# Kernel optimization log

Measured on AMD Instinct MI355X. Metric: run time of the kernel, lower is better.

Reference implementation:

```python
import jax, jax.numpy as jnp
import numpy as np

B, S, H, D = 2, 4096, 16, 128  # batch, seq, heads, head_dim
HID = H * D                    # 2048 hidden size
C = 128                        # chunk size for the chunked recurrent scan
EPS = 1e-6


def setup_inputs() -> dict:
    key = jax.random.key(0)
    ks = jax.random.split(key, 9)
    sc = 0.02  # initializer_range
    w = lambda k: jax.random.normal(k, (HID, HID), jnp.float32) * sc
    return {
        "x": jax.random.normal(ks[0], (B, S, HID), jnp.float32),
        "Wq": w(ks[1]), "bq": jnp.zeros((HID,), jnp.float32),
        "Wk": w(ks[2]), "bk": jnp.zeros((HID,), jnp.float32),
        "Wv": w(ks[3]), "bv": jnp.zeros((HID,), jnp.float32),
        "Wo": w(ks[4]), "bo": jnp.zeros((HID,), jnp.float32),
    }


def reference(x, Wq, bq, Wk, bk, Wv, bv, Wo, bo):
    Bx, Sx, hid = x.shape
    NC = Sx // C  # number of chunks

    q = (x @ Wq + bq).reshape(Bx, Sx, H, D)
    k = (x @ Wk + bk).reshape(Bx, Sx, H, D)
    v = (x @ Wv + bv).reshape(Bx, Sx, H, D)

    # positive feature map for linear attention
    qf = jax.nn.elu(q) + 1.0
    kf = jax.nn.elu(k) + 1.0

    # chunk: [B, NC, C, H, D]
    qf = qf.reshape(Bx, NC, C, H, D)
    kf = kf.reshape(Bx, NC, C, H, D)
    vc = v.reshape(Bx, NC, C, H, D)

    # inter-chunk recurrent state: exclusive cumulative sums of per-chunk KV outer
    kv = jnp.einsum('bnchd,bnche->bnhde', kf, vc)      # per-chunk KV state
    kv_ex = jnp.cumsum(kv, axis=1) - kv                # exclusive prefix state
    ksum = kf.sum(axis=2)                              # [B,NC,H,D]
    ksum_ex = jnp.cumsum(ksum, axis=1) - ksum          # exclusive normalizer state

    inter = jnp.einsum('bnchd,bnhde->bnche', qf, kv_ex)
    z_inter = jnp.einsum('bnchd,bnhd->bnch', qf, ksum_ex)

    # intra-chunk causal attention (masked matmul)
    A = jnp.einsum('bnchd,bnkhd->bnhck', qf, kf)       # [B,NC,H,C,C]
    causal = jnp.tril(jnp.ones((C, C), dtype=bool))
    A = jnp.where(causal[None, None, None], A, 0.0)
    intra = jnp.einsum('bnhck,bnkhe->bnche', A, vc)
    z_intra = jnp.swapaxes(A.sum(-1), 2, 3)            # [B,NC,C,H]

    out = (inter + intra) / (z_inter + z_intra + EPS)[..., None]
    out = out.reshape(Bx, Sx, hid)
    return out @ Wo + bo
```

## Files before the change

### kernel.cpp

```cpp
#include <hip/hip_runtime.h>

typedef unsigned short u16;
typedef unsigned int u32;
typedef unsigned long long u64;
typedef __attribute__((ext_vector_type(8))) short short8;
typedef __attribute__((ext_vector_type(4))) float f32x4;
typedef __attribute__((ext_vector_type(4))) int int4v;

constexpr int Bsz = 2, Ssz = 4096, Hn = 16, Dh = 128, HID = 2048;
constexpr int Cch = 128, NCh = 32;
constexpr float EPSf = 1e-6f;

#define MFMA16 __builtin_amdgcn_mfma_f32_16x16x32_bf16
#define VMW(N) asm volatile("s_waitcnt vmcnt(" #N ")" ::: "memory")

__device__ __forceinline__ float b2f(u16 u) {
  unsigned int i = ((unsigned int)u) << 16;
  return __builtin_bit_cast(float, i);
}
__device__ __forceinline__ u16 f2b(float f) {
  unsigned int i = __builtin_bit_cast(unsigned int, f);
  i += 0x7fffu + ((i >> 16) & 1u);
  return (u16)(i >> 16);
}

__device__ __forceinline__ void gload_lds16(const u16* g, u16* l) {
  __builtin_amdgcn_global_load_lds(
      (const __attribute__((address_space(1))) u32*)g,
      (__attribute__((address_space(3))) u32*)l, 16, 0, 0);
}

__global__ __launch_bounds__(256) void cvt_bf16(const float* __restrict__ x,
                                                u16* __restrict__ xb)
{
  const size_t n8 = (size_t)Bsz * Ssz * HID / 8;
  for (size_t i = (size_t)blockIdx.x * 256 + threadIdx.x; i < n8;
       i += (size_t)gridDim.x * 256) {
    const f32x4 a = *(const f32x4*)&x[i * 8];
    const f32x4 b = *(const f32x4*)&x[i * 8 + 4];
    u16 tmp[8];
#pragma unroll
    for (int u = 0; u < 4; ++u) { tmp[u] = f2b(a[u]); tmp[u + 4] = f2b(b[u]); }
    *(int4v*)&xb[i * 8] = *(const int4v*)tmp;
  }
}

__global__ __launch_bounds__(256) void transpose4(
    const float* __restrict__ A0, const float* __restrict__ A1,
    const float* __restrict__ A2, const float* __restrict__ A3,
    u16* __restrict__ T0, u16* __restrict__ T1,
    u16* __restrict__ T2, u16* __restrict__ T3)
{
  constexpr int N = HID, LDT = 72;
  const int z = blockIdx.z;
  const float* __restrict__ A = (z == 0) ? A0 : (z == 1) ? A1 : (z == 2) ? A2 : A3;
  u16* __restrict__ T = (z == 0) ? T0 : (z == 1) ? T1 : (z == 2) ? T2 : T3;
  __shared__ u16 lds[64 * LDT];
  const int t = threadIdx.x;
  const int i = t >> 3, j = (t & 7) * 8;
  const int r0 = blockIdx.y * 64, c0 = blockIdx.x * 64;
#pragma unroll
  for (int half = 0; half < 2; ++half) {
    const int r = i + half * 32;
    const f32x4 a = *(const f32x4*)&A[(size_t)(r0 + r) * N + c0 + j];
    const f32x4 b = *(const f32x4*)&A[(size_t)(r0 + r) * N + c0 + j + 4];
    u16 tmp[8];
#pragma unroll
    for (int u = 0; u < 4; ++u) { tmp[u] = f2b(a[u]); tmp[u + 4] = f2b(b[u]); }
    *(int4v*)&lds[r * LDT + j] = *(const int4v*)tmp;
  }
  __syncthreads();
#pragma unroll
  for (int half = 0; half < 2; ++half) {
    const int c = i + half * 32;
    u16 tmp[8];
#pragma unroll
    for (int u = 0; u < 8; ++u) tmp[u] = lds[(j + u) * LDT + c];
    *(int4v*)&T[(size_t)(c0 + c) * N + r0 + j] = *(const int4v*)tmp;
  }
}

template <int OUTF32>
__global__ __launch_bounds__(512) void gemm4b(
    const u16* __restrict__ A,
    const u16* __restrict__ W0T, const u16* __restrict__ W1T, const u16* __restrict__ W2T,
    const float* __restrict__ bb0, const float* __restrict__ bb1, const float* __restrict__ bb2,
    void* __restrict__ o0, void* __restrict__ o1, void* __restrict__ o2,
    int elu_mask)
{
  constexpr int K = HID, N = HID;
  extern __shared__ u16 lds[];

  const int z = blockIdx.z;
  const u16* __restrict__ WT    = (z == 0) ? W0T : (z == 1) ? W1T : W2T;
  const float* __restrict__ bias = (z == 0) ? bb0 : (z == 1) ? bb1 : bb2;
  void* __restrict__ outv = (z == 0) ? o0 : (z == 1) ? o1 : o2;
  const bool elu = (elu_mask >> z) & 1;

  const int lid = blockIdx.x + 8 * blockIdx.y;
  const int k8 = lid & 7, j32 = lid >> 3;
  const int m0 = (k8 * 4 + (j32 >> 3)) * 256;
  const int n0 = (j32 & 7) * 256;

  const int t = threadIdx.x, lane = t & 63, w = t >> 6;
  const int wm = w >> 2, wn = w & 3;
  const int l15 = lane & 15, lg = lane >> 4;
  const int sl2 = (l15 >> 1) & 3;

  const int strow = lane >> 2;
  const int stslot = (lane & 3) ^ ((lane >> 3) & 3);
  const u16* gA = A  + (size_t)(m0 + w * 16 + strow) * K + stslot * 8;
  const u16* gB = WT + (size_t)(n0 + w * 16 + strow) * K + stslot * 8;

  const int aRow = (wm * 128 + l15) * 32 + ((lg ^ sl2) << 3);
  const int bRow = 8192 + (wn * 64 + l15) * 32 + ((lg ^ sl2) << 3);
  u16* const lw = &lds[w * 512];

  f32x4 acc[8][4] = {};
  short8 aF[8], bF[4];

#define STAGE4(SB) do {                                                       \
    gload_lds16(gA,                   lw + (SB)*16384);                       \
    gload_lds16(gA + (size_t)128*K,   lw + (SB)*16384 + 4096);                \
    gload_lds16(gB,                   lw + (SB)*16384 + 8192);                \
    gload_lds16(gB + (size_t)128*K,   lw + (SB)*16384 + 8192 + 4096);         \
    gA += 32; gB += 32;                                                       \
  } while (0)

#define WINDOW(BUF, SB, PF, VMN) do {                                         \
    VMW(VMN);                                                                 \
    __builtin_amdgcn_s_barrier();                                             \
    if (PF) STAGE4(SB);                                                       \
    _Pragma("unroll")                                                         \
    for (int i = 0; i < 8; ++i)                                               \
      aF[i] = *(const short8*)&lds[(BUF)*16384 + aRow + i*512];               \
    _Pragma("unroll")                                                         \
    for (int j = 0; j < 4; ++j)                                               \
      bF[j] = *(const short8*)&lds[(BUF)*16384 + bRow + j*512];               \
    __builtin_amdgcn_s_setprio(1);                                            \
    _Pragma("unroll")                                                         \
    for (int i = 0; i < 8; ++i) {                                             \
      acc[i][0] = MFMA16(aF[i], bF[0], acc[i][0], 0, 0, 0);                   \
      acc[i][1] = MFMA16(aF[i], bF[1], acc[i][1], 0, 0, 0);                   \
      acc[i][2] = MFMA16(aF[i], bF[2], acc[i][2], 0, 0, 0);                   \
      acc[i][3] = MFMA16(aF[i], bF[3], acc[i][3], 0, 0, 0);                   \
    }                                                                         \
    __builtin_amdgcn_s_setprio(0);                                            \
  } while (0)

  STAGE4(0);
  STAGE4(1);
  STAGE4(2);

  for (int W = 0; W < 60; W += 4) {
    WINDOW(0, 3, 1, 8);
    WINDOW(1, 0, 1, 8);
    WINDOW(2, 1, 1, 8);
    WINDOW(3, 2, 1, 8);
  }
  WINDOW(0, 3, 1, 8);
  WINDOW(1, 0, 0, 8);
  WINDOW(2, 0, 0, 4);
  WINDOW(3, 0, 0, 0);

  if (OUTF32) {
#pragma unroll
    for (int j = 0; j < 4; ++j) {
      const int col = n0 + wn * 64 + j * 16 + l15;
      const float bv = bias[col];
#pragma unroll
      for (int i = 0; i < 8; ++i) {
        const int row0 = m0 + wm * 128 + i * 16 + lg * 4;
#pragma unroll
        for (int r = 0; r < 4; ++r) {
          float v = acc[i][j][r] + bv;
          if (elu) v = (v > 0.0f) ? (v + 1.0f) : __expf(v);
          ((float*)outv)[(size_t)(row0 + r) * N + col] = v;
        }
      }
    }
  } else {
    __builtin_amdgcn_s_barrier();
    u16* const myr = &lds[w * 8192];
#pragma unroll
    for (int j = 0; j < 4; ++j) {
      const float bv = bias[n0 + wn * 64 + j * 16 + l15];
#pragma unroll
      for (int i = 0; i < 8; ++i)
#pragma unroll
        for (int r = 0; r < 4; ++r) {
          float v = acc[i][j][r] + bv;
          if (elu) v = (v > 0.0f) ? (v + 1.0f) : __expf(v);
          myr[(i * 16 + lg * 4 + r) * 64 + j * 16 + l15] = f2b(v);
        }
    }
    const int rl = lane >> 3, ch = (lane & 7) * 8;
    u16* const og = (u16*)outv + (size_t)(m0 + wm * 128) * N + n0 + wn * 64;
#pragma unroll
    for (int si = 0; si < 16; ++si) {
      const int rw = si * 8 + rl;
      *(int4v*)&og[(size_t)rw * N + ch] = *(const int4v*)&myr[rw * 64 + ch];
    }
  }
#undef STAGE4
#undef WINDOW
}

__global__ __launch_bounds__(256) void pass1_kv(
    const u16* __restrict__ KF, const u16* __restrict__ V,
    u16* __restrict__ KVT, float* __restrict__ KSUM)
{
  constexpr int LD = 136;
  __shared__ u16 lk[128 * LD];
  __shared__ u16 lv[128 * LD];
  __shared__ float kp[256];
  const int bnh = blockIdx.x;
  const int h = bnh % Hn, n = (bnh / Hn) % NCh, b = bnh / (Hn * NCh);
  const size_t rowbase = (size_t)(b * Ssz + n * Cch) * HID + h * Dh;
  const int t = threadIdx.x, lane = t & 63, w = t >> 6;
  const int wr = (w >> 1) * 64, wc = (w & 1) * 64;
  const int l15 = lane & 15, lg = lane >> 4;
  const int sr = t >> 4, sc = (t & 15) * 8;

#pragma unroll
  for (int rep = 0; rep < 8; ++rep) {
    const int r = rep * 16 + sr;
    *(int4v*)&lk[r * LD + sc] = *(const int4v*)&KF[rowbase + (size_t)r * HID + sc];
    *(int4v*)&lv[r * LD + sc] = *(const int4v*)&V[rowbase + (size_t)r * HID + sc];
  }
  __syncthreads();

  {
    const int col = t & 127, hf = t >> 7;
    float s = 0.0f;
    for (int c = hf * 64; c < hf * 64 + 64; ++c) s += b2f(lk[c * LD + col]);
    kp[t] = s;
  }
  __syncthreads();
  if (t < 128) KSUM[(size_t)bnh * Dh + t] = kp[t] + kp[t + 128];

  f32x4 acc[4][4] = {};
#pragma unroll
  for (int kk = 0; kk < 4; ++kk) {
    const int cb = kk * 32 + lg * 8;
    short8 aF[4], bF[4];
#pragma unroll
    for (int i = 0; i < 4; ++i) {
      const int e = wr + i * 16 + l15;
      short8 a;
#pragma unroll
      for (int u = 0; u < 8; ++u) a[u] = (short)lv[(cb + u) * LD + e];
      aF[i] = a;
    }
#pragma unroll
    for (int j = 0; j < 4; ++j) {
      const int d = wc + j * 16 + l15;
      short8 bb;
#pragma unroll
      for (int u = 0; u < 8; ++u) bb[u] = (short)lk[(cb + u) * LD + d];
      bF[j] = bb;
    }
#pragma unroll
    for (int i = 0; i < 4; ++i)
#pragma unroll
      for (int j = 0; j < 4; ++j)
        acc[i][j] = MFMA16(aF[i], bF[j], acc[i][j], 0, 0, 0);
  }

  u16* __restrict__ outp = KVT + (size_t)bnh * (Dh * Dh);
#pragma unroll
  for (int i = 0; i < 4; ++i) {
    const int e0 = wr + i * 16 + lg * 4;
#pragma unroll
    for (int j = 0; j < 4; ++j) {
      const int d = wc + j * 16 + l15;
#pragma unroll
      for (int r = 0; r < 4; ++r)
        outp[(size_t)(e0 + r) * Dh + d] = f2b(acc[i][j][r]);
    }
  }
}

__global__ __launch_bounds__(256) void cumsum_all(u16* __restrict__ KVT,
                                                  float* __restrict__ KS)
{
  const int nkv = (Bsz * Hn * Dh * Dh) / 256;
  if ((int)blockIdx.x < nkv) {
    const int tid = blockIdx.x * 256 + threadIdx.x;
    const int ed = tid & (Dh * Dh - 1);
    const int bh = tid >> 14;
    const int h = bh % Hn, b = bh / Hn;
    const size_t base = ((size_t)(b * NCh * Hn) + h) * (Dh * Dh) + ed;
    const size_t stride = (size_t)Hn * Dh * Dh;
    float s = 0.0f;
    for (int n = 0; n < NCh; ++n) {
      const size_t idx = base + (size_t)n * stride;
      const float v = b2f(KVT[idx]);
      KVT[idx] = f2b(s);
      s += v;
    }
  } else {
    const int tid = (blockIdx.x - nkv) * 256 + threadIdx.x;
    const int d = tid & (Dh - 1);
    const int bh = tid >> 7;
    const int h = bh % Hn, b = bh / Hn;
    const size_t base = ((size_t)(b * NCh * Hn) + h) * Dh + d;
    const size_t stride = (size_t)Hn * Dh;
    float s = 0.0f;
    for (int n = 0; n < NCh; ++n) {
      const size_t idx = base + (size_t)n * stride;
      const float v = KS[idx];
      KS[idx] = s;
      s += v;
    }
  }
}

__global__ __launch_bounds__(256) void pass2_attn(
    const u16* __restrict__ QF, const u16* __restrict__ KF, const u16* __restrict__ V,
    const u16* __restrict__ KVT, const float* __restrict__ KSE,
    u16* __restrict__ Y)
{
  constexpr int LD = 136;
  __shared__ u16 smem[4 * 128 * LD];
  __shared__ float zpart[2][128];
  u16* sQ  = smem;
  u16* sK  = smem + 128 * LD;
  u16* sA  = smem + 2 * 128 * LD;
  u16* sKV = smem + 3 * 128 * LD;

  const int bnh = blockIdx.x;
  const int h = bnh % Hn, n = (bnh / Hn) % NCh, b = bnh / (Hn * NCh);
  const size_t rowbase = (size_t)(b * Ssz + n * Cch) * HID + h * Dh;
  const int t = threadIdx.x, lane = t & 63, w = t >> 6;
  const int wr = (w >> 1) * 64, wc = (w & 1) * 64;
  const int l15 = lane & 15, lg = lane >> 4;
  const int sr = t >> 4, sc = (t & 15) * 8;

  const u16* __restrict__ kvsrc = KVT + (size_t)bnh * (Dh * Dh);
#pragma unroll
  for (int rep = 0; rep < 8; ++rep) {
    const int r = rep * 16 + sr;
    *(int4v*)&sQ[r * LD + sc]  = *(const int4v*)&QF[rowbase + (size_t)r * HID + sc];
    *(int4v*)&sK[r * LD + sc]  = *(const int4v*)&KF[rowbase + (size_t)r * HID + sc];
    *(int4v*)&sKV[r * LD + sc] = *(const int4v*)&kvsrc[r * Dh + sc];
  }
  __syncthreads();

  f32x4 acc[4][4] = {};
#pragma unroll
  for (int kk = 0; kk < 4; ++kk) {
    const int krd = kk * 32 + lg * 8;
    short8 aF[4], bF[4];
#pragma unroll
    for (int i = 0; i < 4; ++i)
      aF[i] = *(const short8*)&sQ[(wr + i * 16 + l15) * LD + krd];
#pragma unroll
    for (int j = 0; j < 4; ++j)
      bF[j] = *(const short8*)&sK[(wc + j * 16 + l15) * LD + krd];
#pragma unroll
    for (int i = 0; i < 4; ++i)
#pragma unroll
      for (int j = 0; j < 4; ++j)
        acc[i][j] = MFMA16(aF[i], bF[j], acc[i][j], 0, 0, 0);
  }
#pragma unroll
  for (int i = 0; i < 4; ++i) {
    const int c0 = wr + i * 16 + lg * 4;
#pragma unroll
    for (int j = 0; j < 4; ++j) {
      const int ck = wc + j * 16 + l15;
#pragma unroll
      for (int r = 0; r < 4; ++r) {
        const int c = c0 + r;
        sA[c * LD + ck] = f2b((ck <= c) ? acc[i][j][r] : 0.0f);
      }
    }
  }
  __syncthreads();

  if (t < 128) {
    const float* kse = KSE + (size_t)bnh * Dh;
    float zz = 0.0f;
    for (int d2 = 0; d2 < 128; d2 += 8) {
      const short8 q8 = *(const short8*)&sQ[t * LD + d2];
      const f32x4 k0 = *(const f32x4*)&kse[d2];
      const f32x4 k1 = *(const f32x4*)&kse[d2 + 4];
      zz += b2f((u16)q8[0]) * k0[0] + b2f((u16)q8[1]) * k0[1]
          + b2f((u16)q8[2]) * k0[2] + b2f((u16)q8[3]) * k0[3]
          + b2f((u16)q8[4]) * k1[0] + b2f((u16)q8[5]) * k1[1]
          + b2f((u16)q8[6]) * k1[2] + b2f((u16)q8[7]) * k1[3];
    }
    zpart[0][t] = zz;
  } else {
    const int row = t - 128;
    float zz = 0.0f;
    for (int ck = 0; ck < 128; ck += 8) {
      const short8 a8 = *(const short8*)&sA[row * LD + ck];
#pragma unroll
      for (int u = 0; u < 8; ++u) zz += b2f((u16)a8[u]);
    }
    zpart[1][row] = zz;
  }
#pragma unroll
  for (int rep = 0; rep < 8; ++rep) {
    const int r = rep * 16 + sr;
    *(int4v*)&sK[r * LD + sc] = *(const int4v*)&V[rowbase + (size_t)r * HID + sc];
  }
  __syncthreads();

  f32x4 o[4][4] = {};
#pragma unroll
  for (int kk = 0; kk < 4; ++kk) {
    const int krd = kk * 32 + lg * 8;
    short8 aF[4], bF[4];
#pragma unroll
    for (int i = 0; i < 4; ++i)
      aF[i] = *(const short8*)&sA[(wr + i * 16 + l15) * LD + krd];
#pragma unroll
    for (int j = 0; j < 4; ++j) {
      const int e = wc + j * 16 + l15;
      short8 bb;
#pragma unroll
      for (int u = 0; u < 8; ++u) bb[u] = (short)sK[(krd + u) * LD + e];
      bF[j] = bb;
    }
#pragma unroll
    for (int i = 0; i < 4; ++i)
#pragma unroll
      for (int j = 0; j < 4; ++j)
        o[i][j] = MFMA16(aF[i], bF[j], o[i][j], 0, 0, 0);
  }
#pragma unroll
  for (int kk = 0; kk < 4; ++kk) {
    const int krd = kk * 32 + lg * 8;
    short8 aF[4], bF[4];
#pragma unroll
    for (int i = 0; i < 4; ++i)
      aF[i] = *(const short8*)&sQ[(wr + i * 16 + l15) * LD + krd];
#pragma unroll
    for (int j = 0; j < 4; ++j)
      bF[j] = *(const short8*)&sKV[(wc + j * 16 + l15) * LD + krd];
#pragma unroll
    for (int i = 0; i < 4; ++i)
#pragma unroll
      for (int j = 0; j < 4; ++j)
        o[i][j] = MFMA16(aF[i], bF[j], o[i][j], 0, 0, 0);
  }

#pragma unroll
  for (int i = 0; i < 4; ++i) {
    const int c0 = wr + i * 16 + lg * 4;
#pragma unroll
    for (int j = 0; j < 4; ++j) {
      const int e = wc + j * 16 + l15;
#pragma unroll
      for (int r = 0; r < 4; ++r) {
        const int c = c0 + r;
        const float zz = zpart[0][c] + zpart[1][c] + EPSf;
        Y[rowbase + (size_t)c * HID + e] = f2b(o[i][j][r] / zz);
      }
    }
  }
}

extern "C" void kernel_launch(void* const* d_in, const int* in_sizes, int n_in,
                              void* d_out, int out_size, void* d_ws, size_t ws_size,
                              hipStream_t stream)
{
  const float* x  = (const float*)d_in[0];
  const float* Wq = (const float*)d_in[1];
  const float* bq = (const float*)d_in[2];
  const float* Wk = (const float*)d_in[3];
  const float* bk = (const float*)d_in[4];
  const float* Wv = (const float*)d_in[5];
  const float* bv = (const float*)d_in[6];
  const float* Wo = (const float*)d_in[7];
  const float* bo = (const float*)d_in[8];
  float* out = (float*)d_out;

  char* p = (char*)d_ws;
  auto take = [&](size_t bytes) { char* q = p; p += (bytes + 255) & ~(size_t)255; return q; };
  u16* WqT = (u16*)take((size_t)HID * HID * 2);
  u16* WkT = (u16*)take((size_t)HID * HID * 2);
  u16* WvT = (u16*)take((size_t)HID * HID * 2);
  u16* WoT = (u16*)take((size_t)HID * HID * 2);
  u16* QF  = (u16*)take((size_t)Bsz * Ssz * HID * 2);
  u16* KFb = (u16*)take((size_t)Bsz * Ssz * HID * 2);
  u16* Vb  = (u16*)take((size_t)Bsz * Ssz * HID * 2);
  char* region = take((size_t)Bsz * Ssz * HID * 2);
  u16* xb  = (u16*)region;
  u16* KVT = (u16*)region;
  float* KS = (float*)take((size_t)Bsz * NCh * Hn * Dh * 4);
  u16* Yb = QF;

  (void)hipFuncSetAttribute((const void*)gemm4b<0>,
                            hipFuncAttributeMaxDynamicSharedMemorySize, 131072);
  (void)hipFuncSetAttribute((const void*)gemm4b<1>,
                            hipFuncAttributeMaxDynamicSharedMemorySize, 131072);

  dim3 blk(256, 1, 1);
  cvt_bf16<<<dim3(2048), blk, 0, stream>>>(x, xb);
  transpose4<<<dim3(HID / 64, HID / 64, 4), blk, 0, stream>>>(
      Wq, Wk, Wv, Wo, WqT, WkT, WvT, WoT);
  gemm4b<0><<<dim3(HID / 256, (Bsz * Ssz) / 256, 3), dim3(512), 131072, stream>>>(
      xb, WqT, WkT, WvT, bq, bk, bv, QF, KFb, Vb, 0x3);
  pass1_kv<<<dim3(Bsz * NCh * Hn), blk, 0, stream>>>(KFb, Vb, KVT, KS);
  cumsum_all<<<dim3((Bsz * Hn * Dh * Dh) / 256 + (Bsz * Hn * Dh) / 256), blk, 0, stream>>>(KVT, KS);
  pass2_attn<<<dim3(Bsz * NCh * Hn), blk, 0, stream>>>(QF, KFb, Vb, KVT, KS, Yb);
  gemm4b<1><<<dim3(HID / 256, (Bsz * Ssz) / 256, 1), dim3(512), 131072, stream>>>(
      Yb, WoT, WoT, WoT, bo, bo, bo, out, out, out, 0);
}
```

Before: 387.3 us.

## Merge prep kernels and stage attention-pass outputs through LDS for coalesced stores

Folds the fp32-to-bf16 input conversion into the weight-transpose kernel as an extra grid slice, removing one launch. In pass1_kv and pass2_attn, MFMA accumulator results are first written to shared memory and then stored to global memory as 16-byte row-contiguous vectors, replacing scattered 2-byte stores. This trades extra barriers and LDS traffic for far fewer, wider global writes.

```diff
diff --git a/kernel.cpp b/kernel.cpp
--- a/kernel.cpp
+++ b/kernel.cpp
@@ -30,22 +30,8 @@
       (__attribute__((address_space(3))) u32*)l, 16, 0, 0);
 }
 
-__global__ __launch_bounds__(256) void cvt_bf16(const float* __restrict__ x,
-                                                u16* __restrict__ xb)
-{
-  const size_t n8 = (size_t)Bsz * Ssz * HID / 8;
-  for (size_t i = (size_t)blockIdx.x * 256 + threadIdx.x; i < n8;
-       i += (size_t)gridDim.x * 256) {
-    const f32x4 a = *(const f32x4*)&x[i * 8];
-    const f32x4 b = *(const f32x4*)&x[i * 8 + 4];
-    u16 tmp[8];
-#pragma unroll
-    for (int u = 0; u < 4; ++u) { tmp[u] = f2b(a[u]); tmp[u + 4] = f2b(b[u]); }
-    *(int4v*)&xb[i * 8] = *(const int4v*)tmp;
-  }
-}
-
-__global__ __launch_bounds__(256) void transpose4(
+__global__ __launch_bounds__(256) void prep(
+    const float* __restrict__ x, u16* __restrict__ xb,
     const float* __restrict__ A0, const float* __restrict__ A1,
     const float* __restrict__ A2, const float* __restrict__ A3,
     u16* __restrict__ T0, u16* __restrict__ T1,
@@ -53,10 +39,25 @@
 {
   constexpr int N = HID, LDT = 72;
   const int z = blockIdx.z;
+  const int t = threadIdx.x;
+
+  if (z == 4) {
+    const size_t n8 = (size_t)Bsz * Ssz * HID / 8;
+    const int bid = blockIdx.y * 32 + blockIdx.x;
+    for (size_t i = (size_t)bid * 256 + t; i < n8; i += (size_t)1024 * 256) {
+      const f32x4 a = *(const f32x4*)&x[i * 8];
+      const f32x4 b = *(const f32x4*)&x[i * 8 + 4];
+      u16 tmp[8];
+#pragma unroll
+      for (int u = 0; u < 4; ++u) { tmp[u] = f2b(a[u]); tmp[u + 4] = f2b(b[u]); }
+      *(int4v*)&xb[i * 8] = *(const int4v*)tmp;
+    }
+    return;
+  }
+
   const float* __restrict__ A = (z == 0) ? A0 : (z == 1) ? A1 : (z == 2) ? A2 : A3;
   u16* __restrict__ T = (z == 0) ? T0 : (z == 1) ? T1 : (z == 2) ? T2 : T3;
   __shared__ u16 lds[64 * LDT];
-  const int t = threadIdx.x;
   const int i = t >> 3, j = (t & 7) * 8;
   const int r0 = blockIdx.y * 64, c0 = blockIdx.x * 64;
 #pragma unroll
@@ -267,7 +268,7 @@
         acc[i][j] = MFMA16(aF[i], bF[j], acc[i][j], 0, 0, 0);
   }
 
-  u16* __restrict__ outp = KVT + (size_t)bnh * (Dh * Dh);
+  __syncthreads();
 #pragma unroll
   for (int i = 0; i < 4; ++i) {
     const int e0 = wr + i * 16 + lg * 4;
@@ -276,8 +277,17 @@
       const int d = wc + j * 16 + l15;
 #pragma unroll
       for (int r = 0; r < 4; ++r)
-        outp[(size_t)(e0 + r) * Dh + d] = f2b(acc[i][j][r]);
-    }
+        lv[(e0 + r) * LD + d] = f2b(acc[i][j][r]);
+    }
+  }
+  __syncthreads();
+  {
+    u16* __restrict__ outp = KVT + (size_t)bnh * (Dh * Dh);
+    const int row = t >> 1, half = (t & 1) * 64;
+#pragma unroll
+    for (int c8 = 0; c8 < 8; ++c8)
+      *(int4v*)&outp[(size_t)row * Dh + half + c8 * 8] =
+          *(const int4v*)&lv[row * LD + half + c8 * 8];
   }
 }
 
@@ -448,6 +458,7 @@
         o[i][j] = MFMA16(aF[i], bF[j], o[i][j], 0, 0, 0);
   }
 
+  __syncthreads();
 #pragma unroll
   for (int i = 0; i < 4; ++i) {
     const int c0 = wr + i * 16 + lg * 4;
@@ -458,9 +469,17 @@
       for (int r = 0; r < 4; ++r) {
         const int c = c0 + r;
         const float zz = zpart[0][c] + zpart[1][c] + EPSf;
-        Y[rowbase + (size_t)c * HID + e] = f2b(o[i][j][r] / zz);
+        sA[c * LD + e] = f2b(o[i][j][r] / zz);
       }
     }
+  }
+  __syncthreads();
+  {
+    const int row = t >> 1, half = (t & 1) * 64;
+#pragma unroll
+    for (int c8 = 0; c8 < 8; ++c8)
+      *(int4v*)&Y[rowbase + (size_t)row * HID + half + c8 * 8] =
+          *(const int4v*)&sA[row * LD + half + c8 * 8];
   }
 }
 
@@ -500,9 +519,8 @@
                             hipFuncAttributeMaxDynamicSharedMemorySize, 131072);
 
   dim3 blk(256, 1, 1);
-  cvt_bf16<<<dim3(2048), blk, 0, stream>>>(x, xb);
-  transpose4<<<dim3(HID / 64, HID / 64, 4), blk, 0, stream>>>(
-      Wq, Wk, Wv, Wo, WqT, WkT, WvT, WoT);
+  prep<<<dim3(32, 32, 5), blk, 0, stream>>>(
+      x, xb, Wq, Wk, Wv, Wo, WqT, WkT, WvT, WoT);
   gemm4b<0><<<dim3(HID / 256, (Bsz * Ssz) / 256, 3), dim3(512), 131072, stream>>>(
       xb, WqT, WkT, WvT, bq, bk, bv, QF, KFb, Vb, 0x3);
   pass1_kv<<<dim3(Bsz * NCh * Hn), blk, 0, stream>>>(KFb, Vb, KVT, KS);
```

After: 398.5 us. 2.9% more time.

## Use 4-wave GEMM blocks with 128x128 per-wave tiles

Applied to the files above, without the earlier changes.

The projection GEMM drops from 8 waves per 256x256 block to 4 waves, each computing a 128x128 sub-tile with 64 accumulators. This doubles register-level reuse of A/B fragments per LDS read and reduces LDS read traffic per MFMA. In exchange, register pressure rises sharply (256 accumulator floats per lane) and there are fewer waves to hide latency, so occupancy drops and spilling is possible.

```diff
diff --git a/kernel.cpp b/kernel.cpp
--- a/kernel.cpp
+++ b/kernel.cpp
@@ -81,7 +81,7 @@
 }
 
 template <int OUTF32>
-__global__ __launch_bounds__(512) void gemm4b(
+__global__ __launch_bounds__(256, 1) void gemm4w(
     const u16* __restrict__ A,
     const u16* __restrict__ W0T, const u16* __restrict__ W1T, const u16* __restrict__ W2T,
     const float* __restrict__ bb0, const float* __restrict__ bb1, const float* __restrict__ bb2,
@@ -103,70 +103,70 @@
   const int n0 = (j32 & 7) * 256;
 
   const int t = threadIdx.x, lane = t & 63, w = t >> 6;
-  const int wm = w >> 2, wn = w & 3;
+  const int wm = w >> 1, wn = w & 1;
   const int l15 = lane & 15, lg = lane >> 4;
   const int sl2 = (l15 >> 1) & 3;
 
   const int strow = lane >> 2;
   const int stslot = (lane & 3) ^ ((lane >> 3) & 3);
-  const u16* gA = A  + (size_t)(m0 + w * 16 + strow) * K + stslot * 8;
-  const u16* gB = WT + (size_t)(n0 + w * 16 + strow) * K + stslot * 8;
+  const u16* gA = A  + (size_t)(m0 + w * 64 + strow) * K + stslot * 8;
+  const u16* gB = WT + (size_t)(n0 + w * 64 + strow) * K + stslot * 8;
 
   const int aRow = (wm * 128 + l15) * 32 + ((lg ^ sl2) << 3);
-  const int bRow = 8192 + (wn * 64 + l15) * 32 + ((lg ^ sl2) << 3);
-  u16* const lw = &lds[w * 512];
-
-  f32x4 acc[8][4] = {};
-  short8 aF[8], bF[4];
-
-#define STAGE4(SB) do {                                                       \
-    gload_lds16(gA,                   lw + (SB)*16384);                       \
-    gload_lds16(gA + (size_t)128*K,   lw + (SB)*16384 + 4096);                \
-    gload_lds16(gB,                   lw + (SB)*16384 + 8192);                \
-    gload_lds16(gB + (size_t)128*K,   lw + (SB)*16384 + 8192 + 4096);         \
+  const int bRow = 8192 + (wn * 128 + l15) * 32 + ((lg ^ sl2) << 3);
+  u16* const lw = &lds[w * 2048];
+
+  f32x4 acc[8][8] = {};
+  short8 aF[8], bF[8];
+
+#define STAGE8(SB) do {                                                       \
+    _Pragma("unroll")                                                         \
+    for (int q = 0; q < 4; ++q)                                               \
+      gload_lds16(gA + (size_t)(q * 16) * K, lw + (SB)*16384 + q * 512);      \
+    _Pragma("unroll")                                                         \
+    for (int q = 0; q < 4; ++q)                                               \
+      gload_lds16(gB + (size_t)(q * 16) * K, lw + (SB)*16384 + 8192 + q * 512);\
     gA += 32; gB += 32;                                                       \
   } while (0)
 
 #define WINDOW(BUF, SB, PF, VMN) do {                                         \
     VMW(VMN);                                                                 \
     __builtin_amdgcn_s_barrier();                                             \
-    if (PF) STAGE4(SB);                                                       \
+    if (PF) STAGE8(SB);                                                       \
     _Pragma("unroll")                                                         \
     for (int i = 0; i < 8; ++i)                                               \
       aF[i] = *(const short8*)&lds[(BUF)*16384 + aRow + i*512];               \
     _Pragma("unroll")                                                         \
-    for (int j = 0; j < 4; ++j)                                               \
+    for (int j = 0; j < 8; ++j)                                               \
       bF[j] = *(const short8*)&lds[(BUF)*16384 + bRow + j*512];               \
     __builtin_amdgcn_s_setprio(1);                                            \
     _Pragma("unroll")                                                         \
-    for (int i = 0; i < 8; ++i) {                                             \
-      acc[i][0] = MFMA16(aF[i], bF[0], acc[i][0], 0, 0, 0);                   \
-      acc[i][1] = MFMA16(aF[i], bF[1], acc[i][1], 0, 0, 0);                   \
-      acc[i][2] = MFMA16(aF[i], bF[2], acc[i][2], 0, 0, 0);                   \
-      acc[i][3] = MFMA16(aF[i], bF[3], acc[i][3], 0, 0, 0);                   \
-    }                                                                         \
+    for (int i = 0; i < 8; ++i)                                               \
+      _Pragma("unroll")                                                       \
+      for (int j = 0; j < 8; ++j)                                             \
+        acc[i][j] = MFMA16(aF[i], bF[j], acc[i][j], 0, 0, 0);                 \
     __builtin_amdgcn_s_setprio(0);                                            \
   } while (0)
 
-  STAGE4(0);
-  STAGE4(1);
-  STAGE4(2);
+  STAGE8(0);
+  STAGE8(1);
+  STAGE8(2);
 
   for (int W = 0; W < 60; W += 4) {
-    WINDOW(0, 3, 1, 8);
-    WINDOW(1, 0, 1, 8);
-    WINDOW(2, 1, 1, 8);
-    WINDOW(3, 2, 1, 8);
-  }
-  WINDOW(0, 3, 1, 8);
-  WINDOW(1, 0, 0, 8);
-  WINDOW(2, 0, 0, 4);
+    WINDOW(0, 3, 1, 16);
+    WINDOW(1, 0, 1, 16);
+    WINDOW(2, 1, 1, 16);
+    WINDOW(3, 2, 1, 16);
+  }
+  WINDOW(0, 3, 1, 16);
+  WINDOW(1, 0, 0, 16);
+  WINDOW(2, 0, 0, 8);
   WINDOW(3, 0, 0, 0);
 
   if (OUTF32) {
 #pragma unroll
-    for (int j = 0; j < 4; ++j) {
-      const int col = n0 + wn * 64 + j * 16 + l15;
+    for (int j = 0; j < 8; ++j) {
+      const int col = n0 + wn * 128 + j * 16 + l15;
       const float bv = bias[col];
 #pragma unroll
       for (int i = 0; i < 8; ++i) {
@@ -181,28 +181,28 @@
     }
   } else {
     __builtin_amdgcn_s_barrier();
-    u16* const myr = &lds[w * 8192];
-#pragma unroll
-    for (int j = 0; j < 4; ++j) {
-      const float bv = bias[n0 + wn * 64 + j * 16 + l15];
+    u16* const myr = &lds[w * 16384];
+#pragma unroll
+    for (int j = 0; j < 8; ++j) {
+      const float bv = bias[n0 + wn * 128 + j * 16 + l15];
 #pragma unroll
       for (int i = 0; i < 8; ++i)
 #pragma unroll
         for (int r = 0; r < 4; ++r) {
           float v = acc[i][j][r] + bv;
           if (elu) v = (v > 0.0f) ? (v + 1.0f) : __expf(v);
-          myr[(i * 16 + lg * 4 + r) * 64 + j * 16 + l15] = f2b(v);
+          myr[(i * 16 + lg * 4 + r) * 128 + j * 16 + l15] = f2b(v);
         }
     }
-    const int rl = lane >> 3, ch = (lane & 7) * 8;
-    u16* const og = (u16*)outv + (size_t)(m0 + wm * 128) * N + n0 + wn * 64;
-#pragma unroll
-    for (int si = 0; si < 16; ++si) {
-      const int rw = si * 8 + rl;
-      *(int4v*)&og[(size_t)rw * N + ch] = *(const int4v*)&myr[rw * 64 + ch];
-    }
-  }
-#undef STAGE4
+    const int rl = lane >> 4, ch = (lane & 15) * 8;
+    u16* const og = (u16*)outv + (size_t)(m0 + wm * 128) * N + n0 + wn * 128;
+#pragma unroll
+    for (int si = 0; si < 32; ++si) {
+      const int rw = si * 4 + rl;
+      *(int4v*)&og[(size_t)rw * N + ch] = *(const int4v*)&myr[rw * 128 + ch];
+    }
+  }
+#undef STAGE8
 #undef WINDOW
 }
 
@@ -494,20 +494,20 @@
   float* KS = (float*)take((size_t)Bsz * NCh * Hn * Dh * 4);
   u16* Yb = QF;
 
-  (void)hipFuncSetAttribute((const void*)gemm4b<0>,
+  (void)hipFuncSetAttribute((const void*)gemm4w<0>,
                             hipFuncAttributeMaxDynamicSharedMemorySize, 131072);
-  (void)hipFuncSetAttribute((const void*)gemm4b<1>,
+  (void)hipFuncSetAttribute((const void*)gemm4w<1>,
                             hipFuncAttributeMaxDynamicSharedMemorySize, 131072);
 
   dim3 blk(256, 1, 1);
   cvt_bf16<<<dim3(2048), blk, 0, stream>>>(x, xb);
   transpose4<<<dim3(HID / 64, HID / 64, 4), blk, 0, stream>>>(
       Wq, Wk, Wv, Wo, WqT, WkT, WvT, WoT);
-  gemm4b<0><<<dim3(HID / 256, (Bsz * Ssz) / 256, 3), dim3(512), 131072, stream>>>(
+  gemm4w<0><<<dim3(HID / 256, (Bsz * Ssz) / 256, 3), blk, 131072, stream>>>(
       xb, WqT, WkT, WvT, bq, bk, bv, QF, KFb, Vb, 0x3);
   pass1_kv<<<dim3(Bsz * NCh * Hn), blk, 0, stream>>>(KFb, Vb, KVT, KS);
   cumsum_all<<<dim3((Bsz * Hn * Dh * Dh) / 256 + (Bsz * Hn * Dh) / 256), blk, 0, stream>>>(KVT, KS);
   pass2_attn<<<dim3(Bsz * NCh * Hn), blk, 0, stream>>>(QF, KFb, Vb, KVT, KS, Yb);
-  gemm4b<1><<<dim3(HID / 256, (Bsz * Ssz) / 256, 1), dim3(512), 131072, stream>>>(
+  gemm4w<1><<<dim3(HID / 256, (Bsz * Ssz) / 256, 1), blk, 131072, stream>>>(
       Yb, WoT, WoT, WoT, bo, bo, bo, out, out, out, 0);
 }
```

Measured after the change: 428.5 us. 10.6% more time.
